# Kernel tuning notes

Measured on AMD Instinct MI355X. Metric: run time of the kernel, lower is better.

## Reference

```python
import jax, jax.numpy as jnp
import numpy as np

B, N, D, NUM_K = 128, 1024, 64, 8


def setup_inputs() -> dict:
    key = jax.random.key(0)
    k1, k2, k3 = jax.random.split(key, 3)
    nodes = jax.random.normal(k1, (B, N, D), dtype=jnp.float32)
    # xavier_uniform over (in_dims, in_dims) fan: bound = sqrt(6 / (N + N))
    bound = float(np.sqrt(6.0 / (N + N)))
    weight = jax.random.uniform(k2, (NUM_K, N, N), dtype=jnp.float32,
                                minval=-bound, maxval=bound)
    graph_shift = jax.random.normal(k3, (N, N), dtype=jnp.float32) / np.sqrt(N)
    return {"nodes": nodes, "weight": weight, "graph_shift": graph_shift}


def reference(nodes, weight, graph_shift):
    """Polynomial graph filter: out[b] = sum_k W_k @ S^k @ X_b.

    Since sum_k W_k S^k X = (sum_k W_k S^k) X, we fuse all taps into one
    N x N operator A, then apply a single batched GEMM over the batch.
    """
    n = nodes.shape[1]
    eye = jnp.eye(n, dtype=nodes.dtype)

    def step(S, Wk):
        # emit W_k @ S^k, carry S^{k+1}
        return S @ graph_shift, Wk @ S

    _, Mk = jax.lax.scan(step, eye, weight)   # [num_k, N, N]
    A = Mk.sum(axis=0)                        # fused filter operator [N, N]
    return jnp.einsum('nm,bmd->bnd', A, nodes)  # [B, N, D]
```

## Files before the change

kernel.cpp:

```cpp
#include <hip/hip_runtime.h>
#include <stdint.h>


#define NN 1024
#define NBATCH 128
#define DDIM 64

typedef float floatx4 __attribute__((ext_vector_type(4)));
typedef _Float16 f16x8 __attribute__((ext_vector_type(8)));
typedef unsigned short u16;

__device__ __forceinline__ u16 f2h(float f) {
  union { _Float16 h; u16 u; } v; v.h = (_Float16)f; return v.u;
}
__device__ __forceinline__ float h2f(u16 u) {
  union { _Float16 h; u16 u; } v; v.u = u; return (float)v.h;
}

__device__ __forceinline__ void gll16(const void* g, void* l) {
  __builtin_amdgcn_global_load_lds(
      (const __attribute__((address_space(1))) void*)g,
      (__attribute__((address_space(3))) void*)l, 16, 0, 0);
}

template <int ROWS>
__device__ __forceinline__ void stage64(const u16* __restrict__ g, u16* lds,
                                        int wave, int lane) {
  const int r = lane >> 3, c = lane & 7;
  const int sw = (c ^ r) * 8;
#pragma unroll
  for (int i = 0; i < ROWS / 32; ++i) {
    const int rb = wave * (ROWS / 4) + i * 8;
    gll16(g + (size_t)(rb + r) * NN + sw, lds + rb * 64);
  }
}

struct CvtJob { const float* src; u16* rm; u16* cm; };
struct CvtJobs { CvtJob j[5]; };

__global__ __launch_bounds__(256) void prep_kernel(CvtJobs jobs,
                                                   const float* __restrict__ X,
                                                   u16* __restrict__ XT) {
  __shared__ u16 T[64][72];
  const int bid = blockIdx.x;
  const int t = threadIdx.x;
  if (bid < 5120) {
    CvtJob jb = jobs.j[bid >> 10];
    int idx4 = (bid & 1023) * 256 + t;
    int e = idx4 * 4;
    int row = e >> 10, col = e & (NN - 1);
    float4 f = ((const float4*)jb.src)[idx4];
    u16 h[4] = { f2h(f.x), f2h(f.y), f2h(f.z), f2h(f.w) };
    uint2 p;
    p.x = (uint32_t)h[0] | ((uint32_t)h[1] << 16);
    p.y = (uint32_t)h[2] | ((uint32_t)h[3] << 16);
    *(uint2*)&jb.rm[e] = p;
    if (jb.cm) {
#pragma unroll
      for (int i = 0; i < 4; ++i) jb.cm[(size_t)(col + i) * NN + row] = h[i];
    }
  } else {
    const int tb = bid - 5120;
    const int k0 = (tb & 15) * 64;
    const int b = tb >> 4;
#pragma unroll
    for (int it = 0; it < 4; ++it) {
      int kr = (t >> 4) + it * 16;
      int d4 = (t & 15) * 4;
      float4 f = *(const float4*)&X[((size_t)b * NN + k0 + kr) * DDIM + d4];
      T[d4 + 0][kr] = f2h(f.x);
      T[d4 + 1][kr] = f2h(f.y);
      T[d4 + 2][kr] = f2h(f.z);
      T[d4 + 3][kr] = f2h(f.w);
    }
    __syncthreads();
#pragma unroll
    for (int it = 0; it < 2; ++it) {
      int d = (t >> 3) + it * 32;
      int kc = (t & 7) * 8;
      *(uint4*)&XT[((size_t)b * DDIM + d) * NN + k0 + kc] = *(uint4*)&T[d][kc];
    }
  }
}

struct GemmJob {
  const u16* A;
  const u16* B;
  const float* addF;
  const u16* addH;
  u16* outRm;
  u16* outCm;
};
struct GemmJobs { GemmJob j[5]; };

template <int BM, int BN, int WM, int WN>
__global__ __launch_bounds__(256) void gemm_f16(GemmJobs jobs) {
  const GemmJob jb = jobs.j[blockIdx.z];
  __shared__ u16 As[2][BM * 64], Bs[2][BN * 64];
  const int t = threadIdx.x, wave = t >> 6, lane = t & 63;
  const int wm = wave / WN, wn = wave % WN;
  const int lm = lane & 15, q = lane >> 4;
  const int bm = blockIdx.x * BM, bn = blockIdx.y * BN;
  constexpr int MI = BM / (WM * 16), NI = BN / (WN * 16);
  floatx4 acc[MI][NI] = {};

  const u16* Ag = jb.A + (size_t)bm * NN;
  const u16* Bg = jb.B + (size_t)bn * NN;

  if (jb.addF) {
#pragma unroll
    for (int mi = 0; mi < MI; ++mi)
#pragma unroll
      for (int ni = 0; ni < NI; ++ni)
#pragma unroll
        for (int r = 0; r < 4; ++r) {
          int row = bm + wm * (BM / WM) + mi * 16 + q * 4 + r;
          int col = bn + wn * (BN / WN) + ni * 16 + lm;
          acc[mi][ni][r] = jb.addF[(size_t)row * NN + col];
        }
  } else if (jb.addH) {
#pragma unroll
    for (int mi = 0; mi < MI; ++mi)
#pragma unroll
      for (int ni = 0; ni < NI; ++ni)
#pragma unroll
        for (int r = 0; r < 4; ++r) {
          int row = bm + wm * (BM / WM) + mi * 16 + q * 4 + r;
          int col = bn + wn * (BN / WN) + ni * 16 + lm;
          acc[mi][ni][r] = h2f(jb.addH[(size_t)row * NN + col]);
        }
  }

  stage64<BM>(Ag, As[0], wave, lane);
  stage64<BN>(Bg, Bs[0], wave, lane);
  __syncthreads();

  for (int kk = 0; kk < 16; ++kk) {
    const int cur = kk & 1;
    if (kk + 1 < 16) {
      stage64<BM>(Ag + (kk + 1) * 64, As[cur ^ 1], wave, lane);
      stage64<BN>(Bg + (kk + 1) * 64, Bs[cur ^ 1], wave, lane);
    }
#pragma unroll
    for (int ks = 0; ks < 2; ++ks) {
      const int st = ((ks * 4 + q) ^ (lm & 7)) * 8;
      f16x8 bf[NI];
#pragma unroll
      for (int ni = 0; ni < NI; ++ni)
        bf[ni] = *(const f16x8*)&Bs[cur][(wn * (BN / WN) + ni * 16 + lm) * 64 + st];
#pragma unroll
      for (int mi = 0; mi < MI; ++mi) {
        f16x8 a = *(const f16x8*)&As[cur][(wm * (BM / WM) + mi * 16 + lm) * 64 + st];
#pragma unroll
        for (int ni = 0; ni < NI; ++ni)
          acc[mi][ni] = __builtin_amdgcn_mfma_f32_16x16x32_f16(a, bf[ni], acc[mi][ni], 0, 0, 0);
      }
    }
    __syncthreads();
  }

#pragma unroll
  for (int mi = 0; mi < MI; ++mi)
#pragma unroll
    for (int ni = 0; ni < NI; ++ni)
#pragma unroll
      for (int r = 0; r < 4; ++r) {
        int row = bm + wm * (BM / WM) + mi * 16 + q * 4 + r;
        int col = bn + wn * (BN / WN) + ni * 16 + lm;
        size_t rm = (size_t)row * NN + col;
        u16 h = f2h(acc[mi][ni][r]);
        if (jb.outRm) jb.outRm[rm] = h;
        if (jb.outCm) jb.outCm[(size_t)col * NN + row] = h;
      }
}

__global__ __launch_bounds__(256) void apply_gemm(const u16* __restrict__ A,
                                                  const u16* __restrict__ XT,
                                                  float* __restrict__ out) {
  __shared__ u16 As[2][128 * 64], Xs[2][128 * 64];
  const int t = threadIdx.x, wave = t >> 6, lane = t & 63;
  const int wm = wave >> 1, wn = wave & 1;
  const int lm = lane & 15, q = lane >> 4;
  const int bn = blockIdx.x * 128;
  const int bm = blockIdx.y * 128;
  floatx4 acc[4][4] = {};
  const u16* Ag = A + (size_t)bm * NN;
  const u16* Xg = XT + (size_t)bn * NN;

  stage64<128>(Ag, As[0], wave, lane);
  stage64<128>(Xg, Xs[0], wave, lane);
  __syncthreads();

  for (int kt = 0; kt < 16; ++kt) {
    const int cur = kt & 1;
    if (kt + 1 < 16) {
      stage64<128>(Ag + (kt + 1) * 64, As[cur ^ 1], wave, lane);
      stage64<128>(Xg + (kt + 1) * 64, Xs[cur ^ 1], wave, lane);
    }
#pragma unroll
    for (int ks = 0; ks < 2; ++ks) {
      const int st = ((ks * 4 + q) ^ (lm & 7)) * 8;
      f16x8 xf[4];
#pragma unroll
      for (int ni = 0; ni < 4; ++ni)
        xf[ni] = *(const f16x8*)&Xs[cur][(wn * 64 + ni * 16 + lm) * 64 + st];
#pragma unroll
      for (int mi = 0; mi < 4; ++mi) {
        f16x8 a = *(const f16x8*)&As[cur][(wm * 64 + mi * 16 + lm) * 64 + st];
#pragma unroll
        for (int ni = 0; ni < 4; ++ni)
          acc[mi][ni] = __builtin_amdgcn_mfma_f32_16x16x32_f16(a, xf[ni], acc[mi][ni], 0, 0, 0);
      }
    }
    __syncthreads();
  }

#pragma unroll
  for (int mi = 0; mi < 4; ++mi)
#pragma unroll
    for (int ni = 0; ni < 4; ++ni)
#pragma unroll
      for (int r = 0; r < 4; ++r) {
        int row = bm + wm * 64 + mi * 16 + q * 4 + r;
        int col = bn + wn * 64 + ni * 16 + lm;
        out[((size_t)(col >> 6) * NN + row) * DDIM + (col & 63)] =
            acc[mi][ni][r];
      }
}

extern "C" void kernel_launch(void* const* d_in, const int* in_sizes, int n_in,
                              void* d_out, int out_size, void* d_ws, size_t ws_size,
                              hipStream_t stream) {
  const float* nodes  = (const float*)d_in[0];
  const float* weight = (const float*)d_in[1];
  const float* gs     = (const float*)d_in[2];
  float* out = (float*)d_out;
  u16* ws = (u16*)d_ws;
  const size_t MB = (size_t)NN * NN;
  auto buf = [&](int i) -> u16* { return ws + (size_t)i * MB; };

  u16* XT = buf(16);
  CvtJobs cv{};
  cv.j[0] = { gs,              buf(0), buf(1) };
  cv.j[1] = { weight + 1 * MB, buf(2), nullptr };
  cv.j[2] = { weight + 3 * MB, buf(3), nullptr };
  cv.j[3] = { weight + 5 * MB, buf(4), nullptr };
  cv.j[4] = { weight + 7 * MB, buf(5), nullptr };
  prep_kernel<<<dim3(5120 + 2048), 256, 0, stream>>>(cv, nodes, XT);

  GemmJobs g1{};
  g1.j[0] = { buf(0), buf(1), nullptr,         nullptr, buf(6),  buf(7)  };
  g1.j[1] = { buf(2), buf(1), weight + 0 * MB, nullptr, buf(8),  nullptr };
  g1.j[2] = { buf(3), buf(1), weight + 2 * MB, nullptr, buf(9),  nullptr };
  g1.j[3] = { buf(4), buf(1), weight + 4 * MB, nullptr, buf(10), nullptr };
  g1.j[4] = { buf(5), buf(1), weight + 6 * MB, nullptr, buf(11), nullptr };
  gemm_f16<64, 128, 2, 2><<<dim3(16, 8, 5), 256, 0, stream>>>(g1);

  GemmJobs g2{};
  g2.j[0] = { buf(6),  buf(7), nullptr, nullptr, nullptr, buf(12) };
  g2.j[1] = { buf(9),  buf(7), nullptr, buf(8),  buf(13), nullptr };
  g2.j[2] = { buf(11), buf(7), nullptr, buf(10), buf(14), nullptr };
  gemm_f16<64, 64, 2, 2><<<dim3(16, 16, 3), 256, 0, stream>>>(g2);

  GemmJobs g3{};
  g3.j[0] = { buf(14), buf(12), nullptr, buf(13), buf(15), nullptr };
  gemm_f16<64, 64, 2, 2><<<dim3(16, 16, 1), 256, 0, stream>>>(g3);

  apply_gemm<<<dim3(64, 8), 256, 0, stream>>>(buf(15), XT, out);
}
```

Measured before the change: 193.6 us.

## Load A fragments directly from global into registers, stage only B in LDS

The operator-building GEMMs now read the A operand straight from global memory into register fragments, double-buffered across k-steps, and stage only the B tile in shared memory. Each wave owns a full-width row slab of 64 columns instead of a 2x2 wave grid. The first GEMM's tiling also changes from 64x128 to 128x64. This removes A's LDS staging and LDS reads and halves shared memory use, at the cost of uncoalesced 16-byte per-lane global loads for A, more register pressure, and less B reuse across waves.

```diff
diff --git a/kernel.cpp b/kernel.cpp
--- a/kernel.cpp
+++ b/kernel.cpp
@@ -93,68 +93,78 @@
 };
 struct GemmJobs { GemmJob j[5]; };
 
-template <int BM, int BN, int WM, int WN>
-__global__ __launch_bounds__(256) void gemm_f16(GemmJobs jobs) {
+template <int BM>
+__global__ __launch_bounds__(256) void gemm_v2(GemmJobs jobs) {
   const GemmJob jb = jobs.j[blockIdx.z];
-  __shared__ u16 As[2][BM * 64], Bs[2][BN * 64];
+  __shared__ u16 Bs[2][64 * 64];
   const int t = threadIdx.x, wave = t >> 6, lane = t & 63;
-  const int wm = wave / WN, wn = wave % WN;
   const int lm = lane & 15, q = lane >> 4;
-  const int bm = blockIdx.x * BM, bn = blockIdx.y * BN;
-  constexpr int MI = BM / (WM * 16), NI = BN / (WN * 16);
-  floatx4 acc[MI][NI] = {};
-
-  const u16* Ag = jb.A + (size_t)bm * NN;
+  const int bm = blockIdx.x * BM, bn = blockIdx.y * 64;
+  constexpr int MI = BM / 64;
+  floatx4 acc[MI][4] = {};
+
   const u16* Bg = jb.B + (size_t)bn * NN;
+  const u16* Ap = jb.A + ((size_t)bm + wave * (BM / 4) + lm) * NN + q * 8;
 
   if (jb.addF) {
 #pragma unroll
     for (int mi = 0; mi < MI; ++mi)
 #pragma unroll
-      for (int ni = 0; ni < NI; ++ni)
+      for (int ni = 0; ni < 4; ++ni)
 #pragma unroll
         for (int r = 0; r < 4; ++r) {
-          int row = bm + wm * (BM / WM) + mi * 16 + q * 4 + r;
-          int col = bn + wn * (BN / WN) + ni * 16 + lm;
+          int row = bm + wave * (BM / 4) + mi * 16 + q * 4 + r;
+          int col = bn + ni * 16 + lm;
           acc[mi][ni][r] = jb.addF[(size_t)row * NN + col];
         }
   } else if (jb.addH) {
 #pragma unroll
     for (int mi = 0; mi < MI; ++mi)
 #pragma unroll
-      for (int ni = 0; ni < NI; ++ni)
+      for (int ni = 0; ni < 4; ++ni)
 #pragma unroll
         for (int r = 0; r < 4; ++r) {
-          int row = bm + wm * (BM / WM) + mi * 16 + q * 4 + r;
-          int col = bn + wn * (BN / WN) + ni * 16 + lm;
+          int row = bm + wave * (BM / 4) + mi * 16 + q * 4 + r;
+          int col = bn + ni * 16 + lm;
           acc[mi][ni][r] = h2f(jb.addH[(size_t)row * NN + col]);
         }
   }
 
-  stage64<BM>(Ag, As[0], wave, lane);
-  stage64<BN>(Bg, Bs[0], wave, lane);
+  f16x8 aF[2][MI * 2];
+  stage64<64>(Bg, Bs[0], wave, lane);
+#pragma unroll
+  for (int mi = 0; mi < MI; ++mi)
+#pragma unroll
+    for (int ks = 0; ks < 2; ++ks)
+      aF[0][mi * 2 + ks] =
+          *(const f16x8*)(Ap + (size_t)mi * 16 * NN + ks * 32);
   __syncthreads();
 
+#pragma unroll
   for (int kk = 0; kk < 16; ++kk) {
     const int cur = kk & 1;
     if (kk + 1 < 16) {
-      stage64<BM>(Ag + (kk + 1) * 64, As[cur ^ 1], wave, lane);
-      stage64<BN>(Bg + (kk + 1) * 64, Bs[cur ^ 1], wave, lane);
+      stage64<64>(Bg + (kk + 1) * 64, Bs[cur ^ 1], wave, lane);
+#pragma unroll
+      for (int mi = 0; mi < MI; ++mi)
+#pragma unroll
+        for (int ks = 0; ks < 2; ++ks)
+          aF[cur ^ 1][mi * 2 + ks] = *(const f16x8*)(
+              Ap + (size_t)mi * 16 * NN + (kk + 1) * 64 + ks * 32);
     }
 #pragma unroll
     for (int ks = 0; ks < 2; ++ks) {
       const int st = ((ks * 4 + q) ^ (lm & 7)) * 8;
-      f16x8 bf[NI];
-#pragma unroll
-      for (int ni = 0; ni < NI; ++ni)
-        bf[ni] = *(const f16x8*)&Bs[cur][(wn * (BN / WN) + ni * 16 + lm) * 64 + st];
-#pragma unroll
-      for (int mi = 0; mi < MI; ++mi) {
-        f16x8 a = *(const f16x8*)&As[cur][(wm * (BM / WM) + mi * 16 + lm) * 64 + st];
-#pragma unroll
-        for (int ni = 0; ni < NI; ++ni)
-          acc[mi][ni] = __builtin_amdgcn_mfma_f32_16x16x32_f16(a, bf[ni], acc[mi][ni], 0, 0, 0);
-      }
+      f16x8 bf[4];
+#pragma unroll
+      for (int ni = 0; ni < 4; ++ni)
+        bf[ni] = *(const f16x8*)&Bs[cur][(ni * 16 + lm) * 64 + st];
+#pragma unroll
+      for (int mi = 0; mi < MI; ++mi)
+#pragma unroll
+        for (int ni = 0; ni < 4; ++ni)
+          acc[mi][ni] = __builtin_amdgcn_mfma_f32_16x16x32_f16(
+              aF[cur][mi * 2 + ks], bf[ni], acc[mi][ni], 0, 0, 0);
     }
     __syncthreads();
   }
@@ -162,11 +172,11 @@
 #pragma unroll
   for (int mi = 0; mi < MI; ++mi)
 #pragma unroll
-    for (int ni = 0; ni < NI; ++ni)
+    for (int ni = 0; ni < 4; ++ni)
 #pragma unroll
       for (int r = 0; r < 4; ++r) {
-        int row = bm + wm * (BM / WM) + mi * 16 + q * 4 + r;
-        int col = bn + wn * (BN / WN) + ni * 16 + lm;
+        int row = bm + wave * (BM / 4) + mi * 16 + q * 4 + r;
+        int col = bn + ni * 16 + lm;
         size_t rm = (size_t)row * NN + col;
         u16 h = f2h(acc[mi][ni][r]);
         if (jb.outRm) jb.outRm[rm] = h;
@@ -254,17 +264,17 @@
   g1.j[2] = { buf(3), buf(1), weight + 2 * MB, nullptr, buf(9),  nullptr };
   g1.j[3] = { buf(4), buf(1), weight + 4 * MB, nullptr, buf(10), nullptr };
   g1.j[4] = { buf(5), buf(1), weight + 6 * MB, nullptr, buf(11), nullptr };
-  gemm_f16<64, 128, 2, 2><<<dim3(16, 8, 5), 256, 0, stream>>>(g1);
+  gemm_v2<128><<<dim3(8, 16, 5), 256, 0, stream>>>(g1);
 
   GemmJobs g2{};
   g2.j[0] = { buf(6),  buf(7), nullptr, nullptr, nullptr, buf(12) };
   g2.j[1] = { buf(9),  buf(7), nullptr, buf(8),  buf(13), nullptr };
   g2.j[2] = { buf(11), buf(7), nullptr, buf(10), buf(14), nullptr };
-  gemm_f16<64, 64, 2, 2><<<dim3(16, 16, 3), 256, 0, stream>>>(g2);
+  gemm_v2<64><<<dim3(16, 16, 3), 256, 0, stream>>>(g2);
 
   GemmJobs g3{};
   g3.j[0] = { buf(14), buf(12), nullptr, buf(13), buf(15), nullptr };
-  gemm_f16<64, 64, 2, 2><<<dim3(16, 16, 1), 256, 0, stream>>>(g3);
+  gemm_v2<64><<<dim3(16, 16, 1), 256, 0, stream>>>(g3);
 
   apply_gemm<<<dim3(64, 8), 256, 0, stream>>>(buf(15), XT, out);
 }
```

After: 200.0 us. 1.03x slower.
